# Kernel optimization log

Measured on AMD Instinct MI355X. Metric: run time of the kernel, lower is better.

## Reference

```python
import jax, jax.numpy as jnp
import numpy as np

EPS = 1e-6
NUM_CLASSES = 100
P_PER_CLASS = 8

def _l2norm(x, axis=-1):
    n = jnp.linalg.norm(x, axis=axis, keepdims=True)
    return x / jnp.maximum(n, EPS)

def setup_inputs() -> dict:
    key = jax.random.key(0)
    k1, k2 = jax.random.split(key)
    feats = jax.random.normal(k1, (64, 768, 32, 32), dtype=jnp.float32)
    prototypes = 0.02 * jax.random.normal(k2, (800, 768), dtype=jnp.float32)
    log_temp = jnp.asarray(np.log(10.0), dtype=jnp.float32)
    return {"feats": feats, "prototypes": prototypes, "log_temp": log_temp}

def reference(feats, prototypes, log_temp):
    B, C, H, W = feats.shape
    tokens = feats.reshape(B, C, H * W).transpose(0, 2, 1)  # [B,T,C]
    tokens_n = _l2norm(tokens)
    protos_n = _l2norm(prototypes)
    temp = jnp.clip(jnp.exp(log_temp), 1e-4, 100.0)
    sim = jnp.einsum('btc,kc->btk', tokens_n, protos_n) * temp  # [B,T,K]
    proto_evidence = jax.nn.logsumexp(sim, axis=1)  # [B,K]
    # proto_class is contiguous blocks of P_PER_CLASS per class -> reshape reduce
    logits = jax.nn.logsumexp(
        proto_evidence.reshape(B, NUM_CLASSES, P_PER_CLASS), axis=-1)
    return logits
```

## Files before the change

### kernel.cpp

```cpp
#include <hip/hip_runtime.h>
#include <hip/hip_bf16.h>

#define B_    64
#define C_    768
#define T_    1024
#define K_    800
#define KPAD  896
#define MT    64
#define NT    128
#define NTILES 7
#define KSTEPS 12
#define NSTEPS 84
#define TCH   16

using bf16x8 = __attribute__((ext_vector_type(8))) short;
using f32x4  = __attribute__((ext_vector_type(4))) float;

__device__ __forceinline__ void gload16(const void* g, void* lds) {
    __builtin_amdgcn_global_load_lds(
        (const __attribute__((address_space(1))) unsigned int*)g,
        (__attribute__((address_space(3))) unsigned int*)lds, 16, 0, 0);
}

__global__ __launch_bounds__(64) void proto_norm_kernel(const float* __restrict__ protos,
                                                        unsigned short* __restrict__ pn) {
    const int row = blockIdx.x;
    const int l = threadIdx.x;
    if (row >= K_) {
        for (int i = 0; i < 12; ++i) pn[(size_t)row * C_ + l + 64 * i] = 0;
        return;
    }
    float v[12];
    float ss = 0.f;
    for (int i = 0; i < 12; ++i) {
        v[i] = protos[(size_t)row * C_ + l + 64 * i];
        ss += v[i] * v[i];
    }
    for (int off = 32; off >= 1; off >>= 1) ss += __shfl_xor(ss, off);
    const float scale = 1.0f / fmaxf(sqrtf(ss), 1e-6f);
    for (int i = 0; i < 12; ++i) {
        __hip_bfloat16 h = __float2bfloat16(v[i] * scale);
        pn[(size_t)row * C_ + l + 64 * i] = *reinterpret_cast<unsigned short*>(&h);
    }
}

__global__ __launch_bounds__(512, 2) void main_kernel(
        const float* __restrict__ feats, const unsigned short* __restrict__ pn,
        const float* __restrict__ log_temp,
        float* __restrict__ wsm, float* __restrict__ wss) {

    __shared__ char  Alds[MT * 1536];
    __shared__ char  Blds[3 * NT * 128];
    __shared__ float ss_lds[MT];
    __shared__ float scale_lds[MT];
    __shared__ float red[8][2][16][2];
    __shared__ float res[NTILES * NT * 2];

    const int tid = threadIdx.x;
    const int l   = tid & 63;
    const int w   = tid >> 6;
    const int g   = l >> 4;
    const int lm  = l & 15;
    const int wm  = w >> 2;
    const int wn  = w & 3;

    const int bb = blockIdx.x >> 4;
    const int tc = blockIdx.x & 15;
    const int t0 = tc * MT;

    const int sSlot8  = (((l & 7) ^ ((l >> 3) & 7))) * 8;
    const int rowLane = (w * 16 + (l >> 3)) * C_ + sSlot8;
    auto stageB = [&](int rowBase, int colOff, int bufi) {
        const unsigned short* gp = pn + rowBase + rowLane + colOff;
        char* lb = &Blds[bufi * 16384 + w * 2048];
        gload16(gp, lb);
        gload16(gp + 8 * C_, lb + 1024);
    };

    stageB(0, 0, 0);
    stageB(0, 64, 1);

    if (tid < MT) ss_lds[tid] = 0.f;
    __syncthreads();

    {
        const int t4 = tid & 15;
        const int cq = tid >> 4;
        float ssp[4] = {0.f, 0.f, 0.f, 0.f};
        const float* fb = feats + (size_t)bb * (C_ * T_) + t0 + t4 * 4;
        #pragma unroll
        for (int i = 0; i < 6; ++i) {
            const int c0 = cq * 4 + i * 128;
            unsigned short hb[4][4];
            #pragma unroll
            for (int j = 0; j < 4; ++j) {
                const float4 v = *reinterpret_cast<const float4*>(fb + (size_t)(c0 + j) * T_);
                const float e[4] = {v.x, v.y, v.z, v.w};
                #pragma unroll
                for (int q = 0; q < 4; ++q) {
                    ssp[q] += e[q] * e[q];
                    __hip_bfloat16 h = __float2bfloat16(e[q]);
                    hb[q][j] = *reinterpret_cast<unsigned short*>(&h);
                }
            }
            #pragma unroll
            for (int q = 0; q < 4; ++q) {
                const int t = t4 * 4 + q;
                unsigned byte = (unsigned)(t * 1536 + c0 * 2);
                byte ^= (unsigned)(((t & 7) ^ ((t >> 3) & 7)) << 4);
                ushort4 pk = {hb[q][0], hb[q][1], hb[q][2], hb[q][3]};
                *reinterpret_cast<ushort4*>(&Alds[byte]) = pk;
            }
        }
        #pragma unroll
        for (int q = 0; q < 4; ++q) {
            ssp[q] += __shfl_xor(ssp[q], 16);
            ssp[q] += __shfl_xor(ssp[q], 32);
        }
        if (l < 16) {
            #pragma unroll
            for (int q = 0; q < 4; ++q) atomicAdd(&ss_lds[l * 4 + q], ssp[q]);
        }
    }
    __syncthreads();
    if (tid < MT) {
        const float temp = fminf(fmaxf(expf(log_temp[0]), 1e-4f), 100.0f);
        scale_lds[tid] = temp / fmaxf(sqrtf(ss_lds[tid]), 1e-6f);
    }
    __syncthreads();

    int bufC = 0;
    int sRB  = 0, sKS = 2;
    const float tsA0 = 0.f; (void)tsA0;

    for (int nt = 0; nt < NTILES; ++nt) {
        f32x4 acc[2][2] = {};

        for (int ks = 0; ks < KSTEPS; ++ks) {
            const int u = nt * KSTEPS + ks;
            if (u < NSTEPS - 1) {
                asm volatile("s_waitcnt vmcnt(2)" ::: "memory");
            } else {
                asm volatile("s_waitcnt vmcnt(0)" ::: "memory");
            }
            __builtin_amdgcn_s_barrier();

            bf16x8 a[2][2], b[2][2];
            #pragma unroll
            for (int kk = 0; kk < 2; ++kk) {
                #pragma unroll
                for (int mi = 0; mi < 2; ++mi) {
                    const int t = wm * 32 + mi * 16 + lm;
                    unsigned byte = (unsigned)(t * 1536 + (ks * 64 + kk * 32 + g * 8) * 2);
                    byte ^= (unsigned)(((t & 7) ^ ((t >> 3) & 7)) << 4);
                    a[kk][mi] = *reinterpret_cast<const bf16x8*>(&Alds[byte]);
                }
                #pragma unroll
                for (int ni = 0; ni < 2; ++ni) {
                    const int n = wn * 32 + ni * 16 + lm;
                    const int j = (kk * 4 + g) ^ (n & 7);
                    b[kk][ni] = *reinterpret_cast<const bf16x8*>(
                        &Blds[bufC * 16384 + n * 128 + j * 16]);
                }
            }

            if (u + 2 < NSTEPS) {
                const int bufS = (bufC == 0) ? 2 : bufC - 1;
                stageB(sRB, sKS * 64, bufS);
                if (++sKS == KSTEPS) { sKS = 0; sRB += NT * C_; }
            }

            __builtin_amdgcn_s_setprio(1);
            #pragma unroll
            for (int kk = 0; kk < 2; ++kk)
                #pragma unroll
                for (int mi = 0; mi < 2; ++mi)
                    #pragma unroll
                    for (int ni = 0; ni < 2; ++ni)
                        acc[mi][ni] = __builtin_amdgcn_mfma_f32_16x16x32_bf16(
                            a[kk][mi], b[kk][ni], acc[mi][ni], 0, 0, 0);
            __builtin_amdgcn_s_setprio(0);

            bufC = (bufC == 2) ? 0 : bufC + 1;
        }

        float4 sc[2];
        #pragma unroll
        for (int mi = 0; mi < 2; ++mi)
            sc[mi] = *reinterpret_cast<const float4*>(&scale_lds[wm * 32 + mi * 16 + g * 4]);

        #pragma unroll
        for (int ni = 0; ni < 2; ++ni) {
            float vals[8];
            float mloc = -3.0e38f;
            #pragma unroll
            for (int mi = 0; mi < 2; ++mi) {
                const float scv[4] = {sc[mi].x, sc[mi].y, sc[mi].z, sc[mi].w};
                #pragma unroll
                for (int r = 0; r < 4; ++r) {
                    const float v = acc[mi][ni][r] * scv[r];
                    vals[mi * 4 + r] = v;
                    mloc = fmaxf(mloc, v);
                }
            }
            float sloc = 0.f;
            #pragma unroll
            for (int i = 0; i < 8; ++i) sloc += expf(vals[i] - mloc);
            #pragma unroll
            for (int off = 16; off <= 32; off <<= 1) {
                const float mo = __shfl_xor(mloc, off);
                const float so = __shfl_xor(sloc, off);
                const float M = fmaxf(mloc, mo);
                sloc = sloc * expf(mloc - M) + so * expf(mo - M);
                mloc = M;
            }
            if (l < 16) { red[w][ni][lm][0] = mloc; red[w][ni][lm][1] = sloc; }
        }
        asm volatile("s_waitcnt lgkmcnt(0)" ::: "memory");
        __builtin_amdgcn_s_barrier();
        if (wm == 0 && l < 16) {
            #pragma unroll
            for (int ni = 0; ni < 2; ++ni) {
                const float m0 = red[w][ni][lm][0],     s0 = red[w][ni][lm][1];
                const float m1 = red[w + 4][ni][lm][0], s1 = red[w + 4][ni][lm][1];
                const float M = fmaxf(m0, m1);
                const float S = s0 * expf(m0 - M) + s1 * expf(m1 - M);
                const int r = nt * NT + wn * 32 + ni * 16 + lm;
                res[r * 2 + 0] = M;
                res[r * 2 + 1] = S;
            }
        }
    }

    asm volatile("s_waitcnt lgkmcnt(0)" ::: "memory");
    __builtin_amdgcn_s_barrier();

    const size_t wsbase = ((size_t)bb * TCH + tc) * KPAD;
    for (int e = tid; e < NTILES * NT; e += 512) {
        wsm[wsbase + e] = res[e * 2 + 0];
        wss[wsbase + e] = res[e * 2 + 1];
    }
}

__global__ __launch_bounds__(128) void final_kernel(const float* __restrict__ wsm,
                                                    const float* __restrict__ wss,
                                                    float* __restrict__ out) {
    const int b = blockIdx.x;
    const int c = threadIdx.x;
    if (c >= 100) return;
    float M = -3.0e38f, S = 0.f;
    for (int ch = 0; ch < TCH; ++ch) {
        const size_t base = ((size_t)b * TCH + ch) * KPAD + c * 8;
        #pragma unroll
        for (int p = 0; p < 8; ++p) {
            const float m = wsm[base + p], s = wss[base + p];
            const float Mn = fmaxf(M, m);
            S = S * expf(M - Mn) + s * expf(m - Mn);
            M = Mn;
        }
    }
    out[b * 100 + c] = M + logf(S);
}

extern "C" void kernel_launch(void* const* d_in, const int* in_sizes, int n_in,
                              void* d_out, int out_size, void* d_ws, size_t ws_size,
                              hipStream_t stream) {
    (void)in_sizes; (void)n_in; (void)out_size; (void)ws_size;
    const float* feats    = (const float*)d_in[0];
    const float* protos   = (const float*)d_in[1];
    const float* log_temp = (const float*)d_in[2];
    float* out = (float*)d_out;

    unsigned short* pn = (unsigned short*)d_ws;
    float* wsm = (float*)((char*)d_ws + (size_t)KPAD * C_ * 2);
    float* wss = wsm + (size_t)B_ * TCH * KPAD;

    proto_norm_kernel<<<KPAD, 64, 0, stream>>>(protos, pn);
    main_kernel<<<B_ * TCH, 512, 0, stream>>>(feats, pn, log_temp, wsm, wss);
    final_kernel<<<B_, 128, 0, stream>>>(wsm, wss, out);
}
```

Before: 436.1 us.

## Split feature normalization into separate kernel and stream A tiles asynchronously

Moves the fp32-to-bf16 conversion and token norm computation into its own kernel. That kernel writes a pre-swizzled bf16 image and per-token scales to workspace. The main GEMM kernel then loads A tiles with async global-to-LDS loads pipelined alongside the B tiles, instead of stalling on a synchronous conversion prologue. The cost is an extra kernel launch plus a write and re-read of about 100MB of bf16 data. Occupancy also drops from 2 blocks to 1 per CU because of the larger LDS footprint.

```diff
diff --git a/kernel.cpp b/kernel.cpp
--- a/kernel.cpp
+++ b/kernel.cpp
@@ -21,6 +21,7 @@
         (const __attribute__((address_space(1))) unsigned int*)g,
         (__attribute__((address_space(3))) unsigned int*)lds, 16, 0, 0);
 }
+__device__ __forceinline__ unsigned swz8(unsigned t) { return (t & 7) ^ ((t >> 3) & 7); }
 
 __global__ __launch_bounds__(64) void proto_norm_kernel(const float* __restrict__ protos,
                                                         unsigned short* __restrict__ pn) {
@@ -44,17 +45,76 @@
     }
 }
 
-__global__ __launch_bounds__(512, 2) void main_kernel(
-        const float* __restrict__ feats, const unsigned short* __restrict__ pn,
-        const float* __restrict__ log_temp,
+__global__ __launch_bounds__(512) void feats_img_kernel(
+        const float* __restrict__ feats, const float* __restrict__ log_temp,
+        unsigned short* __restrict__ img, float* __restrict__ scale) {
+    __shared__ char  A[98304];
+    __shared__ float ss[64];
+    const int tid = threadIdx.x;
+    const int bb = blockIdx.x >> 4, tc = blockIdx.x & 15;
+    const int t0 = tc * 64;
+    if (tid < 64) ss[tid] = 0.f;
+    __syncthreads();
+
+    const int t4 = tid & 15;
+    const int cq = tid >> 4;
+    float ssp[4] = {0.f, 0.f, 0.f, 0.f};
+    const float* fb = feats + (size_t)bb * (C_ * T_) + t0 + t4 * 4;
+    #pragma unroll
+    for (int i = 0; i < 6; ++i) {
+        const int c0 = cq * 4 + i * 128;
+        unsigned short hb[4][4];
+        #pragma unroll
+        for (int j = 0; j < 4; ++j) {
+            const float4 v = *reinterpret_cast<const float4*>(fb + (size_t)(c0 + j) * T_);
+            const float e[4] = {v.x, v.y, v.z, v.w};
+            #pragma unroll
+            for (int q = 0; q < 4; ++q) {
+                ssp[q] += e[q] * e[q];
+                __hip_bfloat16 h = __float2bfloat16(e[q]);
+                hb[q][j] = *reinterpret_cast<unsigned short*>(&h);
+            }
+        }
+        const int ks = c0 >> 6, cc = (c0 >> 3) & 7, half = (c0 >> 2) & 1;
+        #pragma unroll
+        for (int q = 0; q < 4; ++q) {
+            const int t = t4 * 4 + q;
+            const unsigned byte = (unsigned)(ks * 8192 + t * 128 + ((cc ^ swz8(t)) << 4) + half * 8);
+            ushort4 pk = {hb[q][0], hb[q][1], hb[q][2], hb[q][3]};
+            *reinterpret_cast<ushort4*>(&A[byte]) = pk;
+        }
+    }
+    #pragma unroll
+    for (int q = 0; q < 4; ++q) {
+        ssp[q] += __shfl_xor(ssp[q], 16);
+        ssp[q] += __shfl_xor(ssp[q], 32);
+    }
+    if ((tid & 63) < 16) {
+        #pragma unroll
+        for (int q = 0; q < 4; ++q) atomicAdd(&ss[(tid & 63) * 4 + q], ssp[q]);
+    }
+    __syncthreads();
+    if (tid < 64) {
+        const float temp = fminf(fmaxf(expf(log_temp[0]), 1e-4f), 100.0f);
+        scale[blockIdx.x * 64 + tid] = temp / fmaxf(sqrtf(ss[tid]), 1e-6f);
+    }
+    unsigned short* ob = img + (size_t)blockIdx.x * 49152;
+    #pragma unroll
+    for (int k = 0; k < 12; ++k) {
+        bf16x8 v = *reinterpret_cast<const bf16x8*>(&A[k * 8192 + tid * 16]);
+        *reinterpret_cast<bf16x8*>(ob + k * 4096 + tid * 8) = v;
+    }
+}
+
+__global__ __launch_bounds__(512, 1) void main_kernel(
+        const unsigned short* __restrict__ img, const unsigned short* __restrict__ pn,
+        const float* __restrict__ scale,
         float* __restrict__ wsm, float* __restrict__ wss) {
 
-    __shared__ char  Alds[MT * 1536];
-    __shared__ char  Blds[3 * NT * 128];
-    __shared__ float ss_lds[MT];
-    __shared__ float scale_lds[MT];
+    __shared__ char  Aim[98304];
+    __shared__ char  Blds[3 * 16384];
     __shared__ float red[8][2][16][2];
-    __shared__ float res[NTILES * NT * 2];
+    __shared__ float res[KPAD * 2];
 
     const int tid = threadIdx.x;
     const int l   = tid & 63;
@@ -63,10 +123,7 @@
     const int lm  = l & 15;
     const int wm  = w >> 2;
     const int wn  = w & 3;
-
-    const int bb = blockIdx.x >> 4;
-    const int tc = blockIdx.x & 15;
-    const int t0 = tc * MT;
+    const int chunk = blockIdx.x;
 
     const int sSlot8  = (((l & 7) ^ ((l >> 3) & 7))) * 8;
     const int rowLane = (w * 16 + (l >> 3)) * C_ + sSlot8;
@@ -76,73 +133,28 @@
         gload16(gp, lb);
         gload16(gp + 8 * C_, lb + 1024);
     };
-
-    stageB(0, 0, 0);
-    stageB(0, 64, 1);
-
-    if (tid < MT) ss_lds[tid] = 0.f;
-    __syncthreads();
-
-    {
-        const int t4 = tid & 15;
-        const int cq = tid >> 4;
-        float ssp[4] = {0.f, 0.f, 0.f, 0.f};
-        const float* fb = feats + (size_t)bb * (C_ * T_) + t0 + t4 * 4;
-        #pragma unroll
-        for (int i = 0; i < 6; ++i) {
-            const int c0 = cq * 4 + i * 128;
-            unsigned short hb[4][4];
-            #pragma unroll
-            for (int j = 0; j < 4; ++j) {
-                const float4 v = *reinterpret_cast<const float4*>(fb + (size_t)(c0 + j) * T_);
-                const float e[4] = {v.x, v.y, v.z, v.w};
-                #pragma unroll
-                for (int q = 0; q < 4; ++q) {
-                    ssp[q] += e[q] * e[q];
-                    __hip_bfloat16 h = __float2bfloat16(e[q]);
-                    hb[q][j] = *reinterpret_cast<unsigned short*>(&h);
-                }
-            }
-            #pragma unroll
-            for (int q = 0; q < 4; ++q) {
-                const int t = t4 * 4 + q;
-                unsigned byte = (unsigned)(t * 1536 + c0 * 2);
-                byte ^= (unsigned)(((t & 7) ^ ((t >> 3) & 7)) << 4);
-                ushort4 pk = {hb[q][0], hb[q][1], hb[q][2], hb[q][3]};
-                *reinterpret_cast<ushort4*>(&Alds[byte]) = pk;
-            }
-        }
-        #pragma unroll
-        for (int q = 0; q < 4; ++q) {
-            ssp[q] += __shfl_xor(ssp[q], 16);
-            ssp[q] += __shfl_xor(ssp[q], 32);
-        }
-        if (l < 16) {
-            #pragma unroll
-            for (int q = 0; q < 4; ++q) atomicAdd(&ss_lds[l * 4 + q], ssp[q]);
-        }
-    }
-    __syncthreads();
-    if (tid < MT) {
-        const float temp = fminf(fmaxf(expf(log_temp[0]), 1e-4f), 100.0f);
-        scale_lds[tid] = temp / fmaxf(sqrtf(ss_lds[tid]), 1e-6f);
-    }
-    __syncthreads();
+    const unsigned short* ib = img + (size_t)chunk * 49152;
+    auto stageA = [&](int ks) {
+        gload16(ib + ks * 4096 + tid * 8, &Aim[ks * 8192 + tid * 16]);
+    };
+
+    const float4 scv0 = *reinterpret_cast<const float4*>(scale + chunk * 64 + wm * 32 + g * 4);
+    const float4 scv1 = *reinterpret_cast<const float4*>(scale + chunk * 64 + wm * 32 + 16 + g * 4);
+
+    stageA(0); stageB(0, 0, 0);
+    stageA(1); stageB(0, 64, 1);
 
     int bufC = 0;
     int sRB  = 0, sKS = 2;
-    const float tsA0 = 0.f; (void)tsA0;
 
     for (int nt = 0; nt < NTILES; ++nt) {
         f32x4 acc[2][2] = {};
 
         for (int ks = 0; ks < KSTEPS; ++ks) {
             const int u = nt * KSTEPS + ks;
-            if (u < NSTEPS - 1) {
-                asm volatile("s_waitcnt vmcnt(2)" ::: "memory");
-            } else {
-                asm volatile("s_waitcnt vmcnt(0)" ::: "memory");
-            }
+            if (u <= 10)      asm volatile("s_waitcnt vmcnt(3)" ::: "memory");
+            else if (u <= 82) asm volatile("s_waitcnt vmcnt(2)" ::: "memory");
+            else              asm volatile("s_waitcnt vmcnt(0)" ::: "memory");
             __builtin_amdgcn_s_barrier();
 
             bf16x8 a[2][2], b[2][2];
@@ -151,9 +163,9 @@
                 #pragma unroll
                 for (int mi = 0; mi < 2; ++mi) {
                     const int t = wm * 32 + mi * 16 + lm;
-                    unsigned byte = (unsigned)(t * 1536 + (ks * 64 + kk * 32 + g * 8) * 2);
-                    byte ^= (unsigned)(((t & 7) ^ ((t >> 3) & 7)) << 4);
-                    a[kk][mi] = *reinterpret_cast<const bf16x8*>(&Alds[byte]);
+                    const unsigned byte =
+                        (unsigned)(ks * 8192 + t * 128 + (((kk * 4 + g) ^ swz8(t)) << 4));
+                    a[kk][mi] = *reinterpret_cast<const bf16x8*>(&Aim[byte]);
                 }
                 #pragma unroll
                 for (int ni = 0; ni < 2; ++ni) {
@@ -164,7 +176,8 @@
                 }
             }
 
-            if (u + 2 < NSTEPS) {
+            if (u + 2 <= 11) stageA(u + 2);
+            if (u + 2 <= 83) {
                 const int bufS = (bufC == 0) ? 2 : bufC - 1;
                 stageB(sRB, sKS * 64, bufS);
                 if (++sKS == KSTEPS) { sKS = 0; sRB += NT * C_; }
@@ -184,18 +197,14 @@
             bufC = (bufC == 2) ? 0 : bufC + 1;
         }
 
-        float4 sc[2];
-        #pragma unroll
-        for (int mi = 0; mi < 2; ++mi)
-            sc[mi] = *reinterpret_cast<const float4*>(&scale_lds[wm * 32 + mi * 16 + g * 4]);
-
         #pragma unroll
         for (int ni = 0; ni < 2; ++ni) {
             float vals[8];
             float mloc = -3.0e38f;
             #pragma unroll
             for (int mi = 0; mi < 2; ++mi) {
-                const float scv[4] = {sc[mi].x, sc[mi].y, sc[mi].z, sc[mi].w};
+                const float4 sc = mi ? scv1 : scv0;
+                const float scv[4] = {sc.x, sc.y, sc.z, sc.w};
                 #pragma unroll
                 for (int r = 0; r < 4; ++r) {
                     const float v = acc[mi][ni][r] * scv[r];
@@ -235,8 +244,8 @@
     asm volatile("s_waitcnt lgkmcnt(0)" ::: "memory");
     __builtin_amdgcn_s_barrier();
 
-    const size_t wsbase = ((size_t)bb * TCH + tc) * KPAD;
-    for (int e = tid; e < NTILES * NT; e += 512) {
+    const size_t wsbase = (size_t)chunk * KPAD;
+    for (int e = tid; e < KPAD; e += 512) {
         wsm[wsbase + e] = res[e * 2 + 0];
         wss[wsbase + e] = res[e * 2 + 1];
     }
@@ -272,10 +281,13 @@
     float* out = (float*)d_out;
 
     unsigned short* pn = (unsigned short*)d_ws;
-    float* wsm = (float*)((char*)d_ws + (size_t)KPAD * C_ * 2);
-    float* wss = wsm + (size_t)B_ * TCH * KPAD;
+    float* wsm   = (float*)((char*)d_ws + (size_t)KPAD * C_ * 2);
+    float* wss   = wsm + (size_t)B_ * TCH * KPAD;
+    float* scale = wss + (size_t)B_ * TCH * KPAD;
+    unsigned short* img = (unsigned short*)((char*)d_ws + (16u << 20));
 
     proto_norm_kernel<<<KPAD, 64, 0, stream>>>(protos, pn);
-    main_kernel<<<B_ * TCH, 512, 0, stream>>>(feats, pn, log_temp, wsm, wss);
+    feats_img_kernel<<<B_ * TCH, 512, 0, stream>>>(feats, log_temp, img, scale);
+    main_kernel<<<B_ * TCH, 512, 0, stream>>>(img, pn, scale, wsm, wss);
     final_kernel<<<B_, 128, 0, stream>>>(wsm, wss, out);
 }
```

New measurement: 503.2 us. 15.4% more time.
